# Kernel optimization log

Hardware: AMD Instinct MI355X
Metric: run time of the kernel (lower is better)

Reference implementation:

```python
import jax, jax.numpy as jnp
import numpy as np

D_MODEL = 1024
NUM_HEADS = 16
HEAD_DIM = D_MODEL // NUM_HEADS


def setup_inputs() -> dict:
    key = jax.random.key(0)
    ks = jax.random.split(key, 5)
    scale = 0.02
    return {
        "x": jax.random.normal(ks[0], (1, 4096, D_MODEL), dtype=jnp.float32),
        "w_qkv": jax.random.normal(ks[1], (D_MODEL, 3 * D_MODEL), dtype=jnp.float32) * scale,
        "b_qkv": jax.random.normal(ks[2], (3 * D_MODEL,), dtype=jnp.float32) * scale,
        "w_out": jax.random.normal(ks[3], (D_MODEL, D_MODEL), dtype=jnp.float32) * scale,
        "b_out": jax.random.normal(ks[4], (D_MODEL,), dtype=jnp.float32) * scale,
    }


def reference(x, w_qkv, b_qkv, w_out, b_out):
    B, S, D = x.shape
    H, Hd = NUM_HEADS, HEAD_DIM
    qkv = x @ w_qkv + b_qkv  # [B,S,3D]
    q, k, v = jnp.split(qkv, 3, axis=-1)
    # [B,H,S,Hd]
    q = q.reshape(B, S, H, Hd).transpose(0, 2, 1, 3)
    k = k.reshape(B, S, H, Hd).transpose(0, 2, 1, 3)
    v = v.reshape(B, S, H, Hd).transpose(0, 2, 1, 3)
    scores = jnp.einsum("bhqd,bhkd->bhqk", q, k) / jnp.sqrt(jnp.float32(Hd))
    causal = jnp.tril(jnp.ones((S, S), dtype=bool))
    scores = jnp.where(causal[None, None, :, :], scores, -jnp.inf)
    attn = jax.nn.softmax(scores, axis=-1)  # dropout_p = 0.0 -> identity
    ctx = jnp.einsum("bhqk,bhkd->bhqd", attn, v)
    ctx = ctx.transpose(0, 2, 1, 3).reshape(B, S, D)
    return ctx @ w_out + b_out
```

## Files before the change

### kernel.cpp

```cpp
#include <hip/hip_runtime.h>

#define S 4096
#define DM 1024
#define NH 16
#define HD 64

typedef __attribute__((ext_vector_type(8))) short bf8;
typedef __attribute__((ext_vector_type(4))) float f4;
typedef __attribute__((ext_vector_type(4))) short s4;

#define MFMA __builtin_amdgcn_mfma_f32_16x16x32_bf16

#define QSCALE 0.18033688011112042f

static __device__ __forceinline__ unsigned short f2b(float f) {
  unsigned int u = __builtin_bit_cast(unsigned int, f);
  u += 0x7fffu + ((u >> 16) & 1u);
  return (unsigned short)(u >> 16);
}
static __device__ __forceinline__ float b2f(unsigned short u) {
  return __builtin_bit_cast(float, (unsigned int)u << 16);
}

static __device__ __forceinline__ void gld_lds(const unsigned short* g, unsigned short* l) {
  __builtin_amdgcn_global_load_lds(
      (const __attribute__((address_space(1))) unsigned int*)g,
      (__attribute__((address_space(3))) unsigned int*)l, 16, 0, 0);
}

__global__ void prep(const float* __restrict__ x, const float* __restrict__ w_qkv,
                     const float* __restrict__ w_out,
                     unsigned short* __restrict__ xb, unsigned short* __restrict__ wqkvT,
                     unsigned short* __restrict__ woutT) {
  __shared__ float tile[64][65];
  int b = blockIdx.x, t = threadIdx.x;
  if (b < 4096) {
    int i = (b * 256 + t) * 4;
    float4 v = *(const float4*)(x + i);
    s4 o;
    o.x = (short)f2b(v.x); o.y = (short)f2b(v.y);
    o.z = (short)f2b(v.z); o.w = (short)f2b(v.w);
    *(s4*)(xb + i) = o;
    return;
  }
  const float* in; unsigned short* out; int R, C, tc, tr;
  if (b < 4096 + 768) { int bb = b - 4096; in = w_qkv; out = wqkvT; R = DM; C = 3 * DM; tc = bb % 48; tr = bb / 48; }
  else                { int bb = b - 4864; in = w_out; out = woutT; R = DM; C = DM;     tc = bb % 16; tr = bb / 16; }
  int c = t & 63, rbase = (t >> 6) * 16;
#pragma unroll
  for (int i = 0; i < 16; i++) {
    int r = rbase + i;
    tile[r][c] = in[(tr * 64 + r) * C + tc * 64 + c];
  }
  __syncthreads();
#pragma unroll
  for (int i = 0; i < 16; i++) {
    int cc = rbase + i;
    out[(tc * 64 + cc) * R + tr * 64 + c] = f2b(tile[c][cc]);
  }
}


__global__ void __launch_bounds__(256, 2) gemm_qkv(const unsigned short* __restrict__ A,
                                                   const unsigned short* __restrict__ Bt,
                                                   const float* __restrict__ bias,
                                                   unsigned short* __restrict__ Qo,
                                                   unsigned short* __restrict__ Ko,
                                                   unsigned short* __restrict__ Vt) {
  __shared__ unsigned short lA[128 * 32];
  __shared__ unsigned short lB[128 * 32];
  int bid = blockIdx.x;
  int nb = bid % 24, mb = bid / 24;
  int m0 = mb * 128, n0 = nb * 128;
  int t = threadIdx.x, w = t >> 6, lane = t & 63;
  int col = lane & 15, quad = lane >> 4;
  int wm = (w >> 1) * 64, wn = (w & 1) * 64;

  int srow = lane >> 2;
  int sphys = lane & 3;

  f4 acc[4][4];
#pragma unroll
  for (int x = 0; x < 4; x++)
#pragma unroll
    for (int y = 0; y < 4; y++) acc[x][y] = (f4){0.f, 0.f, 0.f, 0.f};

  for (int k0 = 0; k0 < DM; k0 += 32) {
    __syncthreads();
#pragma unroll
    for (int p = 0; p < 2; p++) {
      int j = 2 * w + p;
      int row = j * 16 + srow;
      int lch = sphys ^ ((srow >> 1) & 3);
      gld_lds(A + (size_t)(m0 + row) * DM + k0 + lch * 8, lA + j * 512);
      gld_lds(Bt + (size_t)(n0 + row) * DM + k0 + lch * 8, lB + j * 512);
    }
    __syncthreads();

    bf8 af[4], bfr[4];
#pragma unroll
    for (int x = 0; x < 4; x++) {
      int rA = wm + x * 16 + col;
      af[x] = *(const bf8*)(lA + rA * 32 + (quad ^ ((col >> 1) & 3)) * 8);
      int rB = wn + x * 16 + col;
      bfr[x] = *(const bf8*)(lB + rB * 32 + (quad ^ ((col >> 1) & 3)) * 8);
    }
#pragma unroll
    for (int x = 0; x < 4; x++)
#pragma unroll
      for (int y = 0; y < 4; y++)
        acc[x][y] = MFMA(af[x], bfr[y], acc[x][y], 0, 0, 0);
  }

#pragma unroll
  for (int x = 0; x < 4; x++) {
    int s0r = m0 + wm + x * 16 + quad * 4;
#pragma unroll
    for (int y = 0; y < 4; y++) {
      f4 a = acc[x][y];
      int n = n0 + wn + y * 16 + col;
      float bv = bias[n];
      if (n < 2048) {
        unsigned short* dst = (n < 1024) ? Qo : Ko;
        float sc = (n < 1024) ? QSCALE : 1.0f;
        int nn = n & 1023;
        int hh = nn >> 6, d = nn & 63;
        unsigned short* pp = dst + ((size_t)hh * S + s0r) * HD + d;
#pragma unroll
        for (int r = 0; r < 4; r++) pp[r * HD] = f2b((a[r] + bv) * sc);
      } else {
        int nn = n - 2048;
        int hh = nn >> 6, d = nn & 63;
        s4 pk;
        pk.x = (short)f2b(a[0] + bv);
        pk.y = (short)f2b(a[1] + bv);
        pk.z = (short)f2b(a[2] + bv);
        pk.w = (short)f2b(a[3] + bv);
        *(s4*)(Vt + ((size_t)hh * HD + d) * S + s0r) = pk;
      }
    }
  }
}

__global__ void __launch_bounds__(256, 2) gemm_out(const unsigned short* __restrict__ A,
                                                   const unsigned short* __restrict__ Bt,
                                                   const float* __restrict__ bias,
                                                   float* __restrict__ out) {
  __shared__ unsigned short lA[128 * 32];
  __shared__ unsigned short lB[128 * 32];
  int bid = blockIdx.x;
  int nb = bid % 8, mb = bid / 8;
  int m0 = mb * 128, n0 = nb * 128;
  int t = threadIdx.x, w = t >> 6, lane = t & 63;
  int col = lane & 15, quad = lane >> 4;
  int wm = (w >> 1) * 64, wn = (w & 1) * 64;

  int srow = lane >> 2;
  int sphys = lane & 3;

  f4 acc[4][4];
#pragma unroll
  for (int x = 0; x < 4; x++)
#pragma unroll
    for (int y = 0; y < 4; y++) acc[x][y] = (f4){0.f, 0.f, 0.f, 0.f};

  for (int k0 = 0; k0 < DM; k0 += 32) {
    __syncthreads();
#pragma unroll
    for (int p = 0; p < 2; p++) {
      int j = 2 * w + p;
      int row = j * 16 + srow;
      int lch = sphys ^ ((srow >> 1) & 3);
      gld_lds(A + (size_t)(m0 + row) * DM + k0 + lch * 8, lA + j * 512);
      gld_lds(Bt + (size_t)(n0 + row) * DM + k0 + lch * 8, lB + j * 512);
    }
    __syncthreads();

    bf8 af[4], bfr[4];
#pragma unroll
    for (int x = 0; x < 4; x++) {
      int rA = wm + x * 16 + col;
      af[x] = *(const bf8*)(lA + rA * 32 + (quad ^ ((col >> 1) & 3)) * 8);
      int rB = wn + x * 16 + col;
      bfr[x] = *(const bf8*)(lB + rB * 32 + (quad ^ ((col >> 1) & 3)) * 8);
    }
#pragma unroll
    for (int x = 0; x < 4; x++)
#pragma unroll
      for (int y = 0; y < 4; y++)
        acc[x][y] = MFMA(af[x], bfr[y], acc[x][y], 0, 0, 0);
  }

#pragma unroll
  for (int x = 0; x < 4; x++) {
    int s0r = m0 + wm + x * 16 + quad * 4;
#pragma unroll
    for (int y = 0; y < 4; y++) {
      f4 a = acc[x][y];
      int n = n0 + wn + y * 16 + col;
      float bv = bias[n];
#pragma unroll
      for (int r = 0; r < 4; r++) out[(size_t)(s0r + r) * DM + n] = a[r] + bv;
    }
  }
}

__global__ void __launch_bounds__(256, 6) attn(const unsigned short* __restrict__ Q,
                                               const unsigned short* __restrict__ K,
                                               const unsigned short* __restrict__ Vt,
                                               unsigned short* __restrict__ slabA,
                                               unsigned short* __restrict__ slabB,
                                               float* __restrict__ lA_g,
                                               float* __restrict__ lB_g) {
  __shared__ unsigned short kbuf[64 * 64];
  __shared__ unsigned short vbuf[64 * 64];
  __shared__ unsigned short pbuf[4 * 16 * 72];

  int bid = blockIdx.x;
  int h = bid / 96;
  int r = 95 - (bid % 96);
  int qb, c0, nst, isB;
  if (r < 32) { qb = r; c0 = 0; nst = r + 1; isB = 0; }
  else {
    int qq = (r - 32) >> 1;
    qb = 32 + qq;
    int half = (r - 32) & 1;
    int ntot = qb + 1, nh = (ntot + 1) >> 1;
    if (half) { c0 = nh; nst = ntot - nh; isB = 1; }
    else      { c0 = 0;  nst = nh;       isB = 0; }
  }
  bool single = (qb < 32);
  int q0blk = qb * 64;
  int t = threadIdx.x, w = t >> 6, lane = t & 63;
  int col = lane & 15, quad = lane >> 4;
  int q0 = q0blk + w * 16;

  const unsigned short* Qh = Q + (size_t)h * S * HD;
  const unsigned short* Kh = K + (size_t)h * S * HD;
  const unsigned short* Vh = Vt + (size_t)h * HD * S;
  unsigned short* pl = pbuf + w * (16 * 72);

  bf8 qf0 = *(const bf8*)(Qh + (q0 + col) * HD + quad * 8);
  bf8 qf1 = *(const bf8*)(Qh + (q0 + col) * HD + 32 + quad * 8);

  f4 o[4];
#pragma unroll
  for (int dt = 0; dt < 4; dt++) o[dt] = (f4){0.f, 0.f, 0.f, 0.f};
  float lsum = 0.f;

  int srow = lane >> 3;
  int sphys = lane & 7;

  for (int s_ = 0; s_ < nst; s_++) {
    int kv0 = (c0 + s_) * 64;
    __syncthreads();
#pragma unroll
    for (int p = 0; p < 2; p++) {
      int j = 2 * w + p;
      int row = j * 8 + srow;
      int lch = sphys ^ (row & 7);
      gld_lds(Kh + (size_t)(kv0 + row) * HD + lch * 8, kbuf + j * 512);
      gld_lds(Vh + (size_t)row * S + kv0 + lch * 8, vbuf + j * 512);
    }
    __syncthreads();

    f4 st[4];
#pragma unroll
    for (int tt = 0; tt < 4; tt++) {
      int kr = tt * 16 + col;
      int sw = col & 7;
      bf8 ka = *(const bf8*)(kbuf + kr * 64 + (quad ^ sw) * 8);
      bf8 kb = *(const bf8*)(kbuf + kr * 64 + ((quad + 4) ^ sw) * 8);
      f4 z = {0.f, 0.f, 0.f, 0.f};
      z = MFMA(ka, qf0, z, 0, 0, 0);
      z = MFMA(kb, qf1, z, 0, 0, 0);
      st[tt] = z;
    }

    if (kv0 + 63 > q0) {
      int q = q0 + col;
#pragma unroll
      for (int tt = 0; tt < 4; tt++)
#pragma unroll
        for (int rr = 0; rr < 4; rr++) {
          int kv = kv0 + tt * 16 + quad * 4 + rr;
          st[tt][rr] = (kv <= q) ? st[tt][rr] : -1e30f;
        }
    }

#pragma unroll
    for (int tt = 0; tt < 4; tt++) {
      float p0 = __builtin_amdgcn_exp2f(st[tt][0]);
      float p1 = __builtin_amdgcn_exp2f(st[tt][1]);
      float p2 = __builtin_amdgcn_exp2f(st[tt][2]);
      float p3 = __builtin_amdgcn_exp2f(st[tt][3]);
      lsum += (p0 + p1) + (p2 + p3);
      s4 pk;
      pk.x = (short)f2b(p0); pk.y = (short)f2b(p1);
      pk.z = (short)f2b(p2); pk.w = (short)f2b(p3);
      *(s4*)((char*)pl + col * 144 + tt * 32 + quad * 8) = pk;
    }

    bf8 pf0 = *(const bf8*)(pl + col * 72 + quad * 8);
    bf8 pf1 = *(const bf8*)(pl + col * 72 + 32 + quad * 8);

#pragma unroll
    for (int dt = 0; dt < 4; dt++) {
      int vr = dt * 16 + col;
      int sw = col & 7;
      bf8 v0 = *(const bf8*)(vbuf + vr * 64 + (quad ^ sw) * 8);
      bf8 v1 = *(const bf8*)(vbuf + vr * 64 + ((quad + 4) ^ sw) * 8);
      o[dt] = MFMA(pf0, v0, o[dt], 0, 0, 0);
      o[dt] = MFMA(pf1, v1, o[dt], 0, 0, 0);
    }
  }

  lsum += __shfl_xor(lsum, 16);
  lsum += __shfl_xor(lsum, 32);

  if (single) {
    float inv = 1.0f / lsum;
    float ir[4];
#pragma unroll
    for (int rr = 0; rr < 4; rr++) ir[rr] = __shfl(inv, quad * 4 + rr);
#pragma unroll
    for (int dt = 0; dt < 4; dt++)
#pragma unroll
      for (int rr = 0; rr < 4; rr++) {
        int row = q0 + quad * 4 + rr;
        slabA[(size_t)row * DM + h * HD + dt * 16 + col] = f2b(o[dt][rr] * ir[rr]);
      }
  } else {
    unsigned short* slab = isB ? slabB : slabA;
    int rowbase = isB ? (q0 - 2048) : q0;
    float* lg = isB ? lB_g : lA_g;
    if (quad == 0) lg[h * S + q0 + col] = lsum;
#pragma unroll
    for (int dt = 0; dt < 4; dt++)
#pragma unroll
      for (int rr = 0; rr < 4; rr++) {
        int row = rowbase + quad * 4 + rr;
        slab[(size_t)row * DM + h * HD + dt * 16 + col] = f2b(o[dt][rr]);
      }
  }
}

__global__ void combine(unsigned short* __restrict__ Ctx,
                        const unsigned short* __restrict__ slabB,
                        const float* __restrict__ lA_g,
                        const float* __restrict__ lB_g) {
  int row = 2048 + blockIdx.x;
  int cc = threadIdx.x * 4;
  int h = cc >> 6;
  s4 a = *(const s4*)(Ctx + (size_t)row * DM + cc);
  s4 b = *(const s4*)(slabB + (size_t)(row - 2048) * DM + cc);
  float l = lA_g[h * S + row] + lB_g[h * S + row];
  float inv = 1.0f / l;
  s4 o;
  o.x = (short)f2b((b2f((unsigned short)a.x) + b2f((unsigned short)b.x)) * inv);
  o.y = (short)f2b((b2f((unsigned short)a.y) + b2f((unsigned short)b.y)) * inv);
  o.z = (short)f2b((b2f((unsigned short)a.z) + b2f((unsigned short)b.z)) * inv);
  o.w = (short)f2b((b2f((unsigned short)a.w) + b2f((unsigned short)b.w)) * inv);
  *(s4*)(Ctx + (size_t)row * DM + cc) = o;
}

extern "C" void kernel_launch(void* const* d_in, const int* in_sizes, int n_in,
                              void* d_out, int out_size, void* d_ws, size_t ws_size,
                              hipStream_t stream) {
  const float* x     = (const float*)d_in[0];
  const float* w_qkv = (const float*)d_in[1];
  const float* b_qkv = (const float*)d_in[2];
  const float* w_out = (const float*)d_in[3];
  const float* b_out = (const float*)d_in[4];
  float* out = (float*)d_out;

  char* ws = (char*)d_ws;
  unsigned short* xb    = (unsigned short*)(ws);
  unsigned short* wqkvT = (unsigned short*)(ws + (size_t)8  * 1048576);
  unsigned short* woutT = (unsigned short*)(ws + (size_t)14 * 1048576);
  unsigned short* Qb    = (unsigned short*)(ws + (size_t)16 * 1048576);
  unsigned short* Kb    = (unsigned short*)(ws + (size_t)24 * 1048576);
  unsigned short* Vtb   = (unsigned short*)(ws + (size_t)32 * 1048576);
  unsigned short* ctx   = (unsigned short*)(ws + (size_t)40 * 1048576);

  unsigned short* slabB = xb;
  float* lA_g = (float*)wqkvT;
  float* lB_g = (float*)(ws + (size_t)8 * 1048576 + 512 * 1024);

  prep<<<5120, 256, 0, stream>>>(x, w_qkv, w_out, xb, wqkvT, woutT);
  gemm_qkv<<<32 * 24, 256, 0, stream>>>(xb, wqkvT, b_qkv, Qb, Kb, Vtb);
  attn<<<NH * 96, 256, 0, stream>>>(Qb, Kb, Vtb, ctx, slabB, lA_g, lB_g);
  combine<<<2048, 256, 0, stream>>>(ctx, slabB, lA_g, lB_g);
  gemm_out<<<32 * 8, 256, 0, stream>>>(ctx, woutT, b_out, out);
}
```

Before: 212.7 us.

## Double-buffer K/V tiles in attention and swizzle the P staging buffer

The attention kernel now keeps two LDS buffers each for K and V. It prefetches the next 64-row KV tile while computing on the current one, so each iteration needs one barrier instead of two. The per-wave P staging buffer drops its padded 72-element row stride for an unpadded 64-element row with an XOR chunk swizzle, meant to avoid LDS bank conflicts without the padding. Double buffering roughly doubles K/V LDS use, so the launch-bounds occupancy hint drops from 6 to 4 blocks, trading occupancy for overlap of global-to-LDS loads with compute.

```diff
diff --git a/kernel.cpp b/kernel.cpp
--- a/kernel.cpp
+++ b/kernel.cpp
@@ -205,16 +205,16 @@
   }
 }
 
-__global__ void __launch_bounds__(256, 6) attn(const unsigned short* __restrict__ Q,
+__global__ void __launch_bounds__(256, 4) attn(const unsigned short* __restrict__ Q,
                                                const unsigned short* __restrict__ K,
                                                const unsigned short* __restrict__ Vt,
                                                unsigned short* __restrict__ slabA,
                                                unsigned short* __restrict__ slabB,
                                                float* __restrict__ lA_g,
                                                float* __restrict__ lB_g) {
-  __shared__ unsigned short kbuf[64 * 64];
-  __shared__ unsigned short vbuf[64 * 64];
-  __shared__ unsigned short pbuf[4 * 16 * 72];
+  __shared__ unsigned short kbuf[2][64 * 64];
+  __shared__ unsigned short vbuf[2][64 * 64];
+  __shared__ unsigned short pbuf[4 * 16 * 64];
 
   int bid = blockIdx.x;
   int h = bid / 96;
@@ -238,7 +238,7 @@
   const unsigned short* Qh = Q + (size_t)h * S * HD;
   const unsigned short* Kh = K + (size_t)h * S * HD;
   const unsigned short* Vh = Vt + (size_t)h * HD * S;
-  unsigned short* pl = pbuf + w * (16 * 72);
+  unsigned short* pl = pbuf + w * (16 * 64);
 
   bf8 qf0 = *(const bf8*)(Qh + (q0 + col) * HD + quad * 8);
   bf8 qf1 = *(const bf8*)(Qh + (q0 + col) * HD + 32 + quad * 8);
@@ -250,27 +250,47 @@
 
   int srow = lane >> 3;
   int sphys = lane & 7;
-
-  for (int s_ = 0; s_ < nst; s_++) {
-    int kv0 = (c0 + s_) * 64;
-    __syncthreads();
+  int sw = col & 7;
+  int cs = col & 7;
+  char* pw = (char*)pl + col * 128 + ((quad & 1) << 3);
+
+  {
+    int kv0 = c0 * 64;
 #pragma unroll
     for (int p = 0; p < 2; p++) {
       int j = 2 * w + p;
       int row = j * 8 + srow;
       int lch = sphys ^ (row & 7);
-      gld_lds(Kh + (size_t)(kv0 + row) * HD + lch * 8, kbuf + j * 512);
-      gld_lds(Vh + (size_t)row * S + kv0 + lch * 8, vbuf + j * 512);
-    }
+      gld_lds(Kh + (size_t)(kv0 + row) * HD + lch * 8, &kbuf[0][j * 512]);
+      gld_lds(Vh + (size_t)row * S + kv0 + lch * 8, &vbuf[0][j * 512]);
+    }
+  }
+
+  for (int s_ = 0; s_ < nst; s_++) {
     __syncthreads();
+    int cur = s_ & 1;
+
+    if (s_ + 1 < nst) {
+      int kv0n = (c0 + s_ + 1) * 64;
+      int nxt = cur ^ 1;
+#pragma unroll
+      for (int p = 0; p < 2; p++) {
+        int j = 2 * w + p;
+        int row = j * 8 + srow;
+        int lch = sphys ^ (row & 7);
+        gld_lds(Kh + (size_t)(kv0n + row) * HD + lch * 8, &kbuf[nxt][j * 512]);
+        gld_lds(Vh + (size_t)row * S + kv0n + lch * 8, &vbuf[nxt][j * 512]);
+      }
+    }
+
+    int kv0 = (c0 + s_) * 64;
 
     f4 st[4];
 #pragma unroll
     for (int tt = 0; tt < 4; tt++) {
       int kr = tt * 16 + col;
-      int sw = col & 7;
-      bf8 ka = *(const bf8*)(kbuf + kr * 64 + (quad ^ sw) * 8);
-      bf8 kb = *(const bf8*)(kbuf + kr * 64 + ((quad + 4) ^ sw) * 8);
+      bf8 ka = *(const bf8*)(&kbuf[cur][kr * 64 + (quad ^ sw) * 8]);
+      bf8 kb = *(const bf8*)(&kbuf[cur][kr * 64 + ((quad + 4) ^ sw) * 8]);
       f4 z = {0.f, 0.f, 0.f, 0.f};
       z = MFMA(ka, qf0, z, 0, 0, 0);
       z = MFMA(kb, qf1, z, 0, 0, 0);
@@ -298,18 +318,17 @@
       s4 pk;
       pk.x = (short)f2b(p0); pk.y = (short)f2b(p1);
       pk.z = (short)f2b(p2); pk.w = (short)f2b(p3);
-      *(s4*)((char*)pl + col * 144 + tt * 32 + quad * 8) = pk;
-    }
-
-    bf8 pf0 = *(const bf8*)(pl + col * 72 + quad * 8);
-    bf8 pf1 = *(const bf8*)(pl + col * 72 + 32 + quad * 8);
+      *(s4*)(pw + (((tt * 2 + (quad >> 1)) ^ cs) << 4)) = pk;
+    }
+
+    bf8 pf0 = *(const bf8*)((char*)pl + col * 128 + (((quad + 0) ^ cs) << 4));
+    bf8 pf1 = *(const bf8*)((char*)pl + col * 128 + (((quad + 4) ^ cs) << 4));
 
 #pragma unroll
     for (int dt = 0; dt < 4; dt++) {
       int vr = dt * 16 + col;
-      int sw = col & 7;
-      bf8 v0 = *(const bf8*)(vbuf + vr * 64 + (quad ^ sw) * 8);
-      bf8 v1 = *(const bf8*)(vbuf + vr * 64 + ((quad + 4) ^ sw) * 8);
+      bf8 v0 = *(const bf8*)(&vbuf[cur][vr * 64 + (quad ^ sw) * 8]);
+      bf8 v1 = *(const bf8*)(&vbuf[cur][vr * 64 + ((quad + 4) ^ sw) * 8]);
       o[dt] = MFMA(pf0, v0, o[dt], 0, 0, 0);
       o[dt] = MFMA(pf1, v1, o[dt], 0, 0, 0);
     }
```

New measurement: 229.1 us. +7.7%, slower.
